# Performance work log

Measured on AMD Instinct MI355X. Metric: run time of the kernel, lower is better.

Reference implementation:

```python
import jax, jax.numpy as jnp
import numpy as np

# Mamba2(d_model=256, headdim=32) defaults: d_state=128, d_conv=4, expand=2, ngroups=1, chunk=256
B, CIN, L = 8, 256, 1024
D_MODEL = CIN
D_INNER = 2 * D_MODEL            # expand=2 -> 512
HEADDIM = 32
NHEADS = D_INNER // HEADDIM      # 16
D_STATE = 128
D_CONV = 4
CONV_DIM = D_INNER + 2 * D_STATE             # 768 (ngroups=1)
D_IN_PROJ = 2 * D_INNER + 2 * D_STATE + NHEADS  # 1296
GN_GROUPS = 8
CHUNK = 256
EPS = 1e-5

def setup_inputs():
    key = jax.random.key(0)
    ks = jax.random.split(key, 8)
    x = jax.random.normal(ks[0], (B, CIN, L), jnp.float32)
    W_in = jax.random.normal(ks[1], (D_IN_PROJ, D_MODEL), jnp.float32) * 0.02
    conv_w = jax.random.normal(ks[2], (CONV_DIM, D_CONV), jnp.float32) * 0.2
    conv_b = jax.random.normal(ks[3], (CONV_DIM,), jnp.float32) * 0.02
    dt = jnp.exp(jax.random.uniform(ks[4], (NHEADS,)) * (jnp.log(0.1) - jnp.log(0.001)) + jnp.log(0.001))
    dt_bias = dt + jnp.log(-jnp.expm1(-dt))   # inverse softplus
    A_log = jnp.log(jax.random.uniform(ks[5], (NHEADS,), minval=1.0, maxval=16.0))
    Dp = jnp.ones((NHEADS,), jnp.float32)
    rms_w = jnp.ones((D_INNER,), jnp.float32)
    W_out = jax.random.normal(ks[6], (D_MODEL, D_INNER), jnp.float32) * 0.02
    gn_w = jnp.ones((CIN,), jnp.float32)
    gn_b = jnp.zeros((CIN,), jnp.float32)
    return dict(x=x, W_in=W_in, conv_w=conv_w, conv_b=conv_b, dt_bias=dt_bias,
                A_log=A_log, Dp=Dp, rms_w=rms_w, W_out=W_out, gn_w=gn_w, gn_b=gn_b)

def segsum(a):
    # a: (..., T) -> (..., T, T) with sum_{j<i<=t} a_i on/below diagonal, -inf above
    T = a.shape[-1]
    cs = jnp.cumsum(a, -1)
    d = cs[..., :, None] - cs[..., None, :]
    mask = jnp.tril(jnp.ones((T, T), bool))
    return jnp.where(mask, d, -jnp.inf)

def ssd(X, A, Bm, Cm):
    # X: (b,l,h,p) already dt-scaled; A: (b,l,h) = dt*A_cont; Bm,Cm: (b,l,n) (ngroups=1)
    b, l, h, p = X.shape
    n = Bm.shape[-1]
    c = l // CHUNK
    X = X.reshape(b, c, CHUNK, h, p)
    A = A.reshape(b, c, CHUNK, h).transpose(0, 3, 1, 2)      # (b,h,c,l)
    Bm = Bm.reshape(b, c, CHUNK, n)
    Cm = Cm.reshape(b, c, CHUNK, n)
    A_cs = jnp.cumsum(A, -1)                                  # (b,h,c,l)
    Lmat = jnp.exp(segsum(A))                                 # (b,h,c,l,l)
    Y_diag = jnp.einsum('bcln,bcsn,bhcls,bcshp->bclhp', Cm, Bm, Lmat, X)
    decay_states = jnp.exp(A_cs[..., -1:] - A_cs)             # (b,h,c,l)
    states = jnp.einsum('bcln,bhcl,bclhp->bchpn', Bm, decay_states, X)
    decay_chunk = jnp.exp(segsum(jnp.pad(A_cs[..., -1], ((0, 0), (0, 0), (1, 0)))))  # (b,h,c+1,c+1)
    states = jnp.concatenate([jnp.zeros_like(states[:, :1]), states], axis=1)        # (b,c+1,h,p,n)
    prev = jnp.einsum('bhzc,bchpn->bzhpn', decay_chunk, states)[:, :-1]              # (b,c,h,p,n)
    Y_off = jnp.einsum('bcln,bchpn,bhcl->bclhp', Cm, prev, jnp.exp(A_cs))
    return (Y_diag + Y_off).reshape(b, l, h, p)

def _forward(x, W_in, conv_w, conv_b, dt_bias, A_log, Dp, rms_w, W_out, gn_w, gn_b):
    u = jnp.transpose(x, (0, 2, 1))                           # (B,L,d_model)
    zxbcdt = u @ W_in.T                                       # (B,L,1296)
    z = zxbcdt[..., :D_INNER]
    xBC = zxbcdt[..., D_INNER:D_INNER + CONV_DIM]
    dt = jax.nn.softplus(zxbcdt[..., D_INNER + CONV_DIM:] + dt_bias)  # (B,L,H)
    # causal depthwise conv1d + SiLU
    xpad = jnp.pad(xBC, ((0, 0), (D_CONV - 1, 0), (0, 0)))
    xconv = conv_b + sum(conv_w[:, k] * xpad[:, k:k + L, :] for k in range(D_CONV))
    xconv = jax.nn.silu(xconv)
    xs = xconv[..., :D_INNER].reshape(B, L, NHEADS, HEADDIM)
    Bm = xconv[..., D_INNER:D_INNER + D_STATE]
    Cm = xconv[..., D_INNER + D_STATE:]
    A = -jnp.exp(A_log)                                       # (H,)
    Y = ssd(dt[..., None] * xs, dt * A, Bm, Cm)               # (B,L,H,P)
    Y = Y + xs * Dp[None, None, :, None]
    # gated RMSNorm (norm_before_gate=False): rmsnorm(y * silu(z)) * weight
    y = Y.reshape(B, L, D_INNER) * jax.nn.silu(z)
    y = y * jax.lax.rsqrt(jnp.mean(y * y, -1, keepdims=True) + EPS) * rms_w
    out = jnp.transpose(y @ W_out.T, (0, 2, 1))               # (B,C,L)
    # GroupNorm(8, C) over (channels_per_group, L)
    og = out.reshape(B, GN_GROUPS, CIN // GN_GROUPS, L)
    mu = og.mean((2, 3), keepdims=True)
    var = og.var((2, 3), keepdims=True)
    out = ((og - mu) * jax.lax.rsqrt(var + EPS)).reshape(B, CIN, L)
    out = out * gn_w[None, :, None] + gn_b[None, :, None]
    return out * jnp.tanh(jax.nn.softplus(out))               # Mish

def reference(x, W_in, conv_w, conv_b, dt_bias, A_log, Dp, rms_w, W_out, gn_w, gn_b):
    return _forward(x, W_in, conv_w, conv_b, dt_bias, A_log, Dp, rms_w, W_out, gn_w, gn_b)
```

## Files before the change

kernel.cpp:

```cpp
#include <hip/hip_runtime.h>
#include <hip/hip_bf16.h>
#include <math.h>

#define B_ 8
#define L_ 1024
#define DM 256
#define DI 512
#define HD 32
#define NH 16
#define DS 128
#define CDIM 768
#define NZX 1280
#define CH 256
#define NC 4
#define M_ (B_*L_)
#define EPSV 1e-5f

typedef short bf16x8 __attribute__((ext_vector_type(8)));
typedef float f32x4 __attribute__((ext_vector_type(4)));

#define OFF_ZX   0
#define SZ_ZX    (M_*NZX/2)
#define OFF_XC   (OFF_ZX+SZ_ZX)
#define SZ_XC    (M_*CDIM/2)
#define OFF_DT   (OFF_XC+SZ_XC)
#define SZ_DT    (M_*NH)
#define OFF_ACS  (OFF_DT+SZ_DT)
#define SZ_ACS   (B_*NC*NH*CH)
#define OFF_S0   (OFF_ACS+SZ_ACS)
#define SZ_S0    (B_*NC*CH*CH/2)
#define OFF_ST   (OFF_S0+SZ_S0)
#define SZ_ST    (B_*NC*NH*HD*DS)
#define OFF_PV   (OFF_ST+SZ_ST)
#define SZ_PV    SZ_ST
#define OFF_Y    (OFF_PV+SZ_PV)
#define SZ_Y     (M_*DI/2)
#define OFF_YNB  (OFF_Y+SZ_Y)
#define SZ_YNB   (M_*DI/2)
#define OFF_XBF  (OFF_YNB+SZ_YNB)
#define SZ_XBF   (M_*DM/2)
#define OFF_WBF  (OFF_XBF+SZ_XBF)
#define SZ_WBF   (1296*DM/2)
#define OFF_WOBF (OFF_WBF+SZ_WBF)
#define SZ_WOBF  (DM*DI/2)
#define OFF_GNP  (OFF_WOBF+SZ_WOBF)
#define SZ_GNP   (64*2)
#define OFF_BT   (OFF_GNP+SZ_GNP)
#define SZ_BT    (32*128*256/2)

__device__ __forceinline__ ushort f2bf(float v) {
  __hip_bfloat16 h = __float2bfloat16(v);
  return *(ushort*)&h;
}
__device__ __forceinline__ float bf2f(ushort u) {
  return __uint_as_float(((unsigned int)u) << 16);
}

__global__ void k_zero_gnp(float2* __restrict__ gnp) {
  gnp[threadIdx.x] = make_float2(0.f, 0.f);
}

__global__ void k_cast(const float* __restrict__ s, ushort* __restrict__ d, int n) {
  int i = blockIdx.x*256 + threadIdx.x;
  if (i < n) d[i] = f2bf(s[i]);
}

__global__ __launch_bounds__(256) void k_cast_x(const float* __restrict__ x,
                                                ushort* __restrict__ xbf) {
  __shared__ float Ts[64][65];
  const int k0 = blockIdx.x*64, l0 = blockIdx.y*64, b = blockIdx.z;
  const int t = threadIdx.x;
  for (int i = t; i < 4096; i += 256) {
    int kk = i>>6, ll = i&63;
    Ts[kk][ll] = x[(size_t)b*DM*L_ + (size_t)(k0+kk)*L_ + l0+ll];
  }
  __syncthreads();
  for (int i = t; i < 4096; i += 256) {
    int mm = i>>6, kk = i&63;
    xbf[(size_t)(b*L_ + l0+mm)*DM + k0+kk] = f2bf(Ts[kk][mm]);
  }
}

__global__ __launch_bounds__(256) void k_xpose(const ushort* __restrict__ xcb,
                                               ushort* __restrict__ dst,
                                               int src_col0, int ncols) {
  __shared__ ushort T[64][66];
  const int c0 = blockIdx.x*64, l0 = blockIdx.y*64, bc = blockIdx.z;
  const int t = threadIdx.x;
  const int base = bc*CH;
  for (int i = t; i < 4096; i += 256) {
    int lr = i>>6, cc = i&63;
    T[lr][cc] = xcb[(size_t)(base+l0+lr)*CDIM + src_col0 + c0+cc];
  }
  __syncthreads();
  for (int i = t; i < 4096; i += 256) {
    int cc = i>>6, lr = i&63;
    dst[((size_t)bc*ncols + c0+cc)*CH + l0+lr] = T[lr][cc];
  }
}

__global__ __launch_bounds__(256) void k_gemm_in_mfma(const ushort* __restrict__ xbf,
                                                      const ushort* __restrict__ wbf,
                                                      ushort* __restrict__ zxb) {
  __shared__ ushort As[128*40];
  __shared__ ushort Bs[64*40];
  const int tid = threadIdx.x;
  const int n0 = blockIdx.x*64, m0 = blockIdx.y*128;
  const int wave = tid>>6, lane = tid&63;
  const int lr = lane&15, quad = lane>>4;
  const int KK = DM;
  f32x4 acc[2][4];
#pragma unroll
  for (int mi=0;mi<2;++mi)
#pragma unroll
    for (int ni=0;ni<4;++ni)
#pragma unroll
      for (int r=0;r<4;++r) acc[mi][ni][r] = 0.f;
  const int srow = tid>>2, sc = tid&3;
  for (int k0 = 0; k0 < KK; k0 += 32) {
    *(uint4*)&As[srow*40 + sc*8]      = *(const uint4*)(xbf + (size_t)(m0+srow)*KK    + k0 + sc*8);
    *(uint4*)&As[(srow+64)*40 + sc*8] = *(const uint4*)(xbf + (size_t)(m0+srow+64)*KK + k0 + sc*8);
    *(uint4*)&Bs[srow*40 + sc*8]      = *(const uint4*)(wbf + (size_t)(n0+srow)*KK    + k0 + sc*8);
    __syncthreads();
    bf16x8 af[2], bfr[4];
    const int ar = wave*32 + lr;
    af[0] = *(const bf16x8*)&As[ar*40 + quad*8];
    af[1] = *(const bf16x8*)&As[(ar+16)*40 + quad*8];
#pragma unroll
    for (int ni=0;ni<4;++ni) bfr[ni] = *(const bf16x8*)&Bs[(ni*16+lr)*40 + quad*8];
#pragma unroll
    for (int mi=0;mi<2;++mi)
#pragma unroll
      for (int ni=0;ni<4;++ni)
        acc[mi][ni] = __builtin_amdgcn_mfma_f32_16x16x32_bf16(af[mi], bfr[ni], acc[mi][ni], 0, 0, 0);
    __syncthreads();
  }
#pragma unroll
  for (int mi=0;mi<2;++mi) {
    int m = m0 + wave*32 + mi*16 + quad*4;
#pragma unroll
    for (int ni=0;ni<4;++ni) {
      int n = n0 + ni*16 + lr;
#pragma unroll
      for (int r=0;r<4;++r) zxb[(size_t)(m+r)*NZX + n] = f2bf(acc[mi][ni][r]);
    }
  }
}

__global__ __launch_bounds__(256) void k_dt_direct(const float* __restrict__ x,
                                                   const float* __restrict__ W,
                                                   const float* __restrict__ dt_bias,
                                                   float* __restrict__ dtb) {
  __shared__ float Xs[256][16];
  __shared__ float Ws[16][257];
  const int t = threadIdx.x;
  const int bm = blockIdx.x*16;
  const int b = bm >> 10, l0 = bm & 1023;
  for (int i = t; i < 4096; i += 256) {
    int h = i>>8, k = i&255;
    Ws[h][k] = W[(size_t)(NZX+h)*DM + k];
  }
  for (int i = t; i < 4096; i += 256) {
    int k = i>>4, li = i&15;
    Xs[k][li] = x[(size_t)b*DM*L_ + (size_t)k*L_ + l0+li];
  }
  __syncthreads();
  const int h = t&15, li = t>>4;
  float acc = 0.f;
#pragma unroll 8
  for (int k = 0; k < 256; ++k) acc += Xs[k][li]*Ws[h][k];
  float v = acc + dt_bias[h];
  dtb[(size_t)bm*NH + t] = (v > 20.f) ? v : log1pf(expf(v));
}

__global__ __launch_bounds__(256) void k_conv(const ushort* __restrict__ zxb,
                                              const float* __restrict__ cw,
                                              const float* __restrict__ cb,
                                              ushort* __restrict__ xcb) {
  const int j = blockIdx.x*256 + threadIdx.x;
  const int l0 = (blockIdx.y*4) & 1023;
  const int mb = (blockIdx.y*4) & ~1023;
  const float4 w = *(const float4*)&cw[j*4];
  const float bias = cb[j];
  float v[7];
#pragma unroll
  for (int i = 0; i < 7; ++i) {
    int ll = l0 - 3 + i;
    v[i] = (ll >= 0) ? bf2f(zxb[(size_t)(mb+ll)*NZX + DI + j]) : 0.f;
  }
#pragma unroll
  for (int i = 0; i < 4; ++i) {
    float a = bias + w.x*v[i] + w.y*v[i+1] + w.z*v[i+2] + w.w*v[i+3];
    a = a / (1.f + expf(-a));
    xcb[(size_t)(mb+l0+i)*CDIM + j] = f2bf(a);
  }
}

__global__ __launch_bounds__(256) void k_s0_mfma(const ushort* __restrict__ xcb,
                                                 ushort* __restrict__ S0b) {
  const int lt = blockIdx.x, st = blockIdx.y, bc = blockIdx.z;
  if (st > lt) return;
  const int base = bc*CH;
  const int t = threadIdx.x;
  const int wave = t>>6, lane = t&63, lr = lane&15, quad = lane>>4;
  const int l = lt*64 + wave*16 + lr;
  f32x4 acc[4];
#pragma unroll
  for (int nt = 0; nt < 4; ++nt)
#pragma unroll
    for (int r = 0; r < 4; ++r) acc[nt][r] = 0.f;
#pragma unroll
  for (int ks = 0; ks < 4; ++ks) {
    bf16x8 af = *(const bf16x8*)(xcb + (size_t)(base+l)*CDIM + (DI+DS) + ks*32 + quad*8);
#pragma unroll
    for (int nt = 0; nt < 4; ++nt) {
      bf16x8 bf = *(const bf16x8*)(xcb + (size_t)(base + st*64 + nt*16 + lr)*CDIM + DI + ks*32 + quad*8);
      acc[nt] = __builtin_amdgcn_mfma_f32_16x16x32_bf16(af, bf, acc[nt], 0, 0, 0);
    }
  }
#pragma unroll
  for (int nt = 0; nt < 4; ++nt)
#pragma unroll
    for (int r = 0; r < 4; ++r)
      S0b[((size_t)bc*CH + lt*64 + wave*16 + quad*4 + r)*CH + st*64 + nt*16 + lr] = f2bf(acc[nt][r]);
}

__global__ __launch_bounds__(256) void k_states_mfma(const ushort* __restrict__ xcb,
                                                     const ushort* __restrict__ btg,
                                                     const float* __restrict__ dtb,
                                                     const float* __restrict__ A_log,
                                                     float* __restrict__ acs_g,
                                                     float* __restrict__ st) {
  __shared__ float acs[CH];
  __shared__ ushort Xw[32][264];
  const int t = threadIdx.x;
  const int bc = blockIdx.x, h = blockIdx.y;
  const int base = bc*CH;
  float dt_t = dtb[(size_t)(base+t)*NH + h];
  float An = -expf(A_log[h]);
  acs[t] = dt_t * An;
  __syncthreads();
  for (int off = 1; off < CH; off <<= 1) {
    float v = (t >= off) ? acs[t-off] : 0.f;
    __syncthreads();
    acs[t] += v;
    __syncthreads();
  }
  float alast = acs[CH-1];
  acs_g[((size_t)bc*NH + h)*CH + t] = acs[t];
  float w = expf(alast - acs[t]) * dt_t;
  {
    const ushort* xp = xcb + (size_t)(base+t)*CDIM + h*HD;
    ushort tmp[32];
    *(uint4*)&tmp[0]  = *(const uint4*)(xp);
    *(uint4*)&tmp[8]  = *(const uint4*)(xp+8);
    *(uint4*)&tmp[16] = *(const uint4*)(xp+16);
    *(uint4*)&tmp[24] = *(const uint4*)(xp+24);
#pragma unroll
    for (int p = 0; p < 32; ++p) Xw[p][t] = f2bf(bf2f(tmp[p]) * w);
  }
  __syncthreads();
  const int wave = t>>6, lane = t&63, lr = lane&15, quad = lane>>4;
  f32x4 acc[2][2];
#pragma unroll
  for (int mt=0;mt<2;++mt)
#pragma unroll
    for (int nt=0;nt<2;++nt)
#pragma unroll
      for (int r=0;r<4;++r) acc[mt][nt][r] = 0.f;
  const ushort* bp = btg + (size_t)bc*DS*CH;
#pragma unroll
  for (int k0 = 0; k0 < CH; k0 += 32) {
    bf16x8 a0 = *(const bf16x8*)&Xw[lr][k0 + quad*8];
    bf16x8 a1 = *(const bf16x8*)&Xw[16+lr][k0 + quad*8];
    bf16x8 b0 = *(const bf16x8*)(bp + (size_t)(wave*32 + lr)*CH + k0 + quad*8);
    bf16x8 b1 = *(const bf16x8*)(bp + (size_t)(wave*32 + 16 + lr)*CH + k0 + quad*8);
    acc[0][0] = __builtin_amdgcn_mfma_f32_16x16x32_bf16(a0, b0, acc[0][0], 0,0,0);
    acc[0][1] = __builtin_amdgcn_mfma_f32_16x16x32_bf16(a0, b1, acc[0][1], 0,0,0);
    acc[1][0] = __builtin_amdgcn_mfma_f32_16x16x32_bf16(a1, b0, acc[1][0], 0,0,0);
    acc[1][1] = __builtin_amdgcn_mfma_f32_16x16x32_bf16(a1, b1, acc[1][1], 0,0,0);
  }
  size_t sb = ((size_t)bc*NH + h)*HD*DS;
#pragma unroll
  for (int mt = 0; mt < 2; ++mt)
#pragma unroll
    for (int nt = 0; nt < 2; ++nt)
#pragma unroll
      for (int r = 0; r < 4; ++r)
        st[sb + (size_t)(mt*16 + quad*4 + r)*DS + wave*32 + nt*16 + lr] = acc[mt][nt][r];
}

__global__ void k_scan(const float* __restrict__ acs_g, const float* __restrict__ st,
                       float* __restrict__ pv) {
  const int b = blockIdx.x, h = blockIdx.y;
  const int t = threadIdx.x;
  float P[16];
#pragma unroll
  for (int i = 0; i < 16; ++i) P[i] = 0.f;
  for (int c = 0; c < NC; ++c) {
    size_t sb = ((size_t)(b*NC+c)*NH + h)*HD*DS;
    float T = acs_g[((size_t)(b*NC+c)*NH + h)*CH + (CH-1)];
    float ec = expf(T);
#pragma unroll
    for (int i = 0; i < 16; ++i) {
      size_t e = sb + (size_t)i*256 + t;
      pv[e] = P[i];
      P[i] = st[e] + ec * P[i];
    }
  }
}

__global__ __launch_bounds__(256) void k_y_mfma(const ushort* __restrict__ xcb,
    const float* __restrict__ dtb, const float* __restrict__ acs_g,
    const ushort* __restrict__ S0b, const float* __restrict__ pv,
    const float* __restrict__ Dp, ushort* __restrict__ Yb) {
  __shared__ ushort Xt[32][280];
  __shared__ float acs[CH];
  __shared__ float dts[CH];
  __shared__ float E8[CH];
  const int t = threadIdx.x;
  const int bc = blockIdx.x, h = blockIdx.y;
  const int base = bc*CH;
  acs[t] = acs_g[((size_t)bc*NH + h)*CH + t];
  dts[t] = dtb[(size_t)(base+t)*NH + h];
  {
    const ushort* xp = xcb + (size_t)(base+t)*CDIM + h*HD;
    ushort tmp[32];
    *(uint4*)&tmp[0]  = *(const uint4*)(xp);
    *(uint4*)&tmp[8]  = *(const uint4*)(xp+8);
    *(uint4*)&tmp[16] = *(const uint4*)(xp+16);
    *(uint4*)&tmp[24] = *(const uint4*)(xp+24);
#pragma unroll
    for (int p = 0; p < 32; ++p) Xt[p][t] = tmp[p];
  }
  __syncthreads();
  E8[t] = expf(acs[t & ~7] - acs[t]) * dts[t];
  __syncthreads();
  const int wave = t>>6, lane = t&63, lr = lane&15, quad = lane>>4;
  f32x4 acc[4][2];
#pragma unroll
  for (int mt=0;mt<4;++mt)
#pragma unroll
    for (int nt=0;nt<2;++nt)
#pragma unroll
      for (int r=0;r<4;++r) acc[mt][nt][r] = 0.f;
  const size_t pb = ((size_t)bc*NH + h)*HD*DS;
#pragma unroll
  for (int ks = 0; ks < 4; ++ks) {
    bf16x8 bfr[2];
#pragma unroll
    for (int nt = 0; nt < 2; ++nt) {
      const float* pp = pv + pb + (size_t)(nt*16+lr)*DS + ks*32 + quad*8;
      float4 v0 = *(const float4*)pp;
      float4 v1 = *(const float4*)(pp+4);
      bf16x8 bb;
      bb[0]=(short)f2bf(v0.x); bb[1]=(short)f2bf(v0.y); bb[2]=(short)f2bf(v0.z); bb[3]=(short)f2bf(v0.w);
      bb[4]=(short)f2bf(v1.x); bb[5]=(short)f2bf(v1.y); bb[6]=(short)f2bf(v1.z); bb[7]=(short)f2bf(v1.w);
      bfr[nt] = bb;
    }
#pragma unroll
    for (int mt = 0; mt < 4; ++mt) {
      int l = wave*64 + mt*16 + lr;
      bf16x8 af = *(const bf16x8*)(xcb + (size_t)(base+l)*CDIM + (DI+DS) + ks*32 + quad*8);
      acc[mt][0] = __builtin_amdgcn_mfma_f32_16x16x32_bf16(af, bfr[0], acc[mt][0], 0,0,0);
      acc[mt][1] = __builtin_amdgcn_mfma_f32_16x16x32_bf16(af, bfr[1], acc[mt][1], 0,0,0);
    }
  }
#pragma unroll
  for (int mt = 0; mt < 4; ++mt)
#pragma unroll
    for (int r = 0; r < 4; ++r) {
      float e = expf(acs[wave*64 + mt*16 + quad*4 + r]);
      acc[mt][0][r] *= e;
      acc[mt][1][r] *= e;
    }
  float al[4];
#pragma unroll
  for (int mt = 0; mt < 4; ++mt) al[mt] = acs[wave*64 + mt*16 + lr];
  const int km3 = 2*wave + 1;
  for (int ks = 0; ks <= km3; ++ks) {
    const int sq = ks*32 + quad*8;
    const float as0 = acs[sq];
    const float4 e0 = *(const float4*)&E8[sq];
    const float4 e1 = *(const float4*)&E8[sq+4];
    const bf16x8 xb0 = *(const bf16x8*)&Xt[lr][sq];
    const bf16x8 xb1 = *(const bf16x8*)&Xt[16+lr][sq];
    const float ev[8] = {e0.x,e0.y,e0.z,e0.w,e1.x,e1.y,e1.z,e1.w};
#pragma unroll
    for (int mt = 0; mt < 4; ++mt) {
      if (ks > ((wave*64 + mt*16 + 15) >> 5)) continue;
      const int l = wave*64 + mt*16 + lr;
      const bf16x8 sb = *(const bf16x8*)(S0b + ((size_t)bc*CH + l)*CH + sq);
      const float el = expf(al[mt] - as0);
      bf16x8 mf;
#pragma unroll
      for (int j = 0; j < 8; ++j) {
        float v = (sq + j <= l) ? bf2f((ushort)sb[j]) * el * ev[j] : 0.f;
        mf[j] = (short)f2bf(v);
      }
      acc[mt][0] = __builtin_amdgcn_mfma_f32_16x16x32_bf16(mf, xb0, acc[mt][0], 0,0,0);
      acc[mt][1] = __builtin_amdgcn_mfma_f32_16x16x32_bf16(mf, xb1, acc[mt][1], 0,0,0);
    }
  }
  const float dph = Dp[h];
#pragma unroll
  for (int mt = 0; mt < 4; ++mt) {
    const int lb = wave*64 + mt*16 + quad*4;
#pragma unroll
    for (int nt = 0; nt < 2; ++nt) {
      const int p = nt*16 + lr;
#pragma unroll
      for (int r = 0; r < 4; ++r) {
        float xv = bf2f(Xt[p][lb+r]);
        Yb[(size_t)(base+lb+r)*DI + h*HD + p] = f2bf(acc[mt][nt][r] + dph*xv);
      }
    }
  }
}

__global__ __launch_bounds__(256) void k_rms(const ushort* __restrict__ zxb,
                                             const ushort* __restrict__ Yb,
                                             const float* __restrict__ rw,
                                             ushort* __restrict__ yn) {
  const int m = blockIdx.x, t = threadIdx.x;
  float z0 = bf2f(zxb[(size_t)m*NZX + t]);
  float z1 = bf2f(zxb[(size_t)m*NZX + t + 256]);
  float y0 = bf2f(Yb[(size_t)m*DI + t])       * z0 / (1.f + expf(-z0));
  float y1 = bf2f(Yb[(size_t)m*DI + t + 256]) * z1 / (1.f + expf(-z1));
  float ss = y0*y0 + y1*y1;
#pragma unroll
  for (int off = 32; off > 0; off >>= 1) ss += __shfl_down(ss, off);
  __shared__ float red[4];
  __shared__ float sinv;
  if ((t & 63) == 0) red[t >> 6] = ss;
  __syncthreads();
  if (t == 0) sinv = rsqrtf((red[0]+red[1]+red[2]+red[3]) * (1.f/DI) + EPSV);
  __syncthreads();
  float inv = sinv;
  yn[(size_t)m*DI + t]       = f2bf(y0 * inv * rw[t]);
  yn[(size_t)m*DI + t + 256] = f2bf(y1 * inv * rw[t+256]);
}

__global__ __launch_bounds__(256) void k_gemm_out_mfma(const ushort* __restrict__ ynbf,
                                                       const ushort* __restrict__ wobf,
                                                       float* __restrict__ outp,
                                                       float2* __restrict__ gnp) {
  __shared__ ushort As[128*40];
  __shared__ ushort Bs[64*40];
  const int tid = threadIdx.x;
  const int n0 = blockIdx.x*64, m0 = blockIdx.y*128;
  const int wave = tid>>6, lane = tid&63;
  const int lr = lane&15, quad = lane>>4;
  const int KK = DI;
  f32x4 acc[2][4];
#pragma unroll
  for (int mi=0;mi<2;++mi)
#pragma unroll
    for (int ni=0;ni<4;++ni)
#pragma unroll
      for (int r=0;r<4;++r) acc[mi][ni][r] = 0.f;
  const int srow = tid>>2, sc = tid&3;
  for (int k0 = 0; k0 < KK; k0 += 32) {
    *(uint4*)&As[srow*40 + sc*8]      = *(const uint4*)(ynbf + (size_t)(m0+srow)*KK    + k0 + sc*8);
    *(uint4*)&As[(srow+64)*40 + sc*8] = *(const uint4*)(ynbf + (size_t)(m0+srow+64)*KK + k0 + sc*8);
    *(uint4*)&Bs[srow*40 + sc*8]      = *(const uint4*)(wobf + (size_t)(n0+srow)*KK    + k0 + sc*8);
    __syncthreads();
    bf16x8 af[2], bfr[4];
    const int ar = wave*32 + lr;
    af[0] = *(const bf16x8*)&As[ar*40 + quad*8];
    af[1] = *(const bf16x8*)&As[(ar+16)*40 + quad*8];
#pragma unroll
    for (int ni=0;ni<4;++ni) bfr[ni] = *(const bf16x8*)&Bs[(ni*16+lr)*40 + quad*8];
#pragma unroll
    for (int mi=0;mi<2;++mi)
#pragma unroll
      for (int ni=0;ni<4;++ni)
        acc[mi][ni] = __builtin_amdgcn_mfma_f32_16x16x32_bf16(af[mi], bfr[ni], acc[mi][ni], 0, 0, 0);
    __syncthreads();
  }
  const int b = m0 >> 10, l0 = m0 & 1023;
  float s0=0.f, ss0=0.f, s1=0.f, ss1=0.f;
#pragma unroll
  for (int mi=0;mi<2;++mi) {
    int lb = l0 + wave*32 + mi*16 + quad*4;
#pragma unroll
    for (int ni=0;ni<4;++ni) {
      int n = n0 + ni*16 + lr;
      float4 v = make_float4(acc[mi][ni][0], acc[mi][ni][1], acc[mi][ni][2], acc[mi][ni][3]);
      *(float4*)&outp[(size_t)b*DM*L_ + (size_t)n*L_ + lb] = v;
      float ps = v.x+v.y+v.z+v.w;
      float pq = v.x*v.x+v.y*v.y+v.z*v.z+v.w*v.w;
      if (ni < 2) { s0 += ps; ss0 += pq; } else { s1 += ps; ss1 += pq; }
    }
  }
#pragma unroll
  for (int off = 32; off > 0; off >>= 1) {
    s0 += __shfl_down(s0, off); ss0 += __shfl_down(ss0, off);
    s1 += __shfl_down(s1, off); ss1 += __shfl_down(ss1, off);
  }
  __shared__ float red[4][4];
  if (lane == 0) { red[wave][0]=s0; red[wave][1]=ss0; red[wave][2]=s1; red[wave][3]=ss1; }
  __syncthreads();
  if (tid == 0) {
    float S0=0,Q0=0,S1=0,Q1=0;
#pragma unroll
    for (int wv2 = 0; wv2 < 4; ++wv2) { S0+=red[wv2][0]; Q0+=red[wv2][1]; S1+=red[wv2][2]; Q1+=red[wv2][3]; }
    int g0 = b*8 + (n0>>5);
    atomicAdd(&gnp[g0].x, S0);   atomicAdd(&gnp[g0].y, Q0);
    atomicAdd(&gnp[g0+1].x, S1); atomicAdd(&gnp[g0+1].y, Q1);
  }
}

__global__ __launch_bounds__(256) void k_gn_apply(const float2* __restrict__ gnp,
                                                  const float* __restrict__ gw,
                                                  const float* __restrict__ gb,
                                                  float* __restrict__ o) {
  const int ch = blockIdx.x & 255, b = blockIdx.x >> 8;
  const int t = threadIdx.x;
  float2 p = gnp[b*8 + (ch>>5)];
  const float mean = p.x * (1.f/(32.f*L_));
  const float var  = p.y * (1.f/(32.f*L_)) - mean*mean;
  const float inv  = rsqrtf(var + EPSV);
  const float w = gw[ch], bb = gb[ch];
  size_t base = (size_t)blockIdx.x * L_;
  float4 v = *(const float4*)&o[base + t*4];
  float r[4] = {v.x, v.y, v.z, v.w};
#pragma unroll
  for (int j = 0; j < 4; ++j) {
    float u = (r[j] - mean) * inv * w + bb;
    float m;
    if (u > 15.f) m = u;
    else {
      float e = expf(u);
      float a = 1.f + e;
      float a2 = a*a;
      m = u * (a2 - 1.f) / (a2 + 1.f);
    }
    r[j] = m;
  }
  *(float4*)&o[base + t*4] = make_float4(r[0], r[1], r[2], r[3]);
}

extern "C" void kernel_launch(void* const* d_in, const int* in_sizes, int n_in,
                              void* d_out, int out_size, void* d_ws, size_t ws_size,
                              hipStream_t stream) {
  const float* x       = (const float*)d_in[0];
  const float* W_in    = (const float*)d_in[1];
  const float* conv_w  = (const float*)d_in[2];
  const float* conv_b  = (const float*)d_in[3];
  const float* dt_bias = (const float*)d_in[4];
  const float* A_log   = (const float*)d_in[5];
  const float* Dp      = (const float*)d_in[6];
  const float* rms_w   = (const float*)d_in[7];
  const float* W_out   = (const float*)d_in[8];
  const float* gn_w    = (const float*)d_in[9];
  const float* gn_b    = (const float*)d_in[10];
  float* out = (float*)d_out;
  float* ws  = (float*)d_ws;

  ushort* zxb   = (ushort*)(ws + OFF_ZX);
  ushort* xcb   = (ushort*)(ws + OFF_XC);
  float*  dtb   = ws + OFF_DT;
  float*  acs   = ws + OFF_ACS;
  ushort* S0b   = (ushort*)(ws + OFF_S0);
  float*  st    = ws + OFF_ST;
  float*  pv    = ws + OFF_PV;
  ushort* Ybb   = (ushort*)(ws + OFF_Y);
  ushort* ynbf  = (ushort*)(ws + OFF_YNB);
  ushort* xbf   = (ushort*)(ws + OFF_XBF);
  ushort* wbf   = (ushort*)(ws + OFF_WBF);
  ushort* wobf  = (ushort*)(ws + OFF_WOBF);
  float2* gnp   = (float2*)(ws + OFF_GNP);
  ushort* btg   = (ushort*)(ws + OFF_BT);

  k_zero_gnp     <<<dim3(1), 64, 0, stream>>>(gnp);
  k_cast_x       <<<dim3(4, 16, 8), 256, 0, stream>>>(x, xbf);
  k_cast         <<<dim3((1296*DM+255)/256), 256, 0, stream>>>(W_in, wbf, 1296*DM);
  k_cast         <<<dim3((DM*DI+255)/256), 256, 0, stream>>>(W_out, wobf, DM*DI);
  k_gemm_in_mfma <<<dim3(NZX/64, M_/128), 256, 0, stream>>>(xbf, wbf, zxb);
  k_dt_direct    <<<dim3(M_/16), 256, 0, stream>>>(x, W_in, dt_bias, dtb);
  k_conv         <<<dim3(3, M_/4), 256, 0, stream>>>(zxb, conv_w, conv_b, xcb);
  k_xpose        <<<dim3(2, 4, B_*NC), 256, 0, stream>>>(xcb, btg, DI, DS);
  k_s0_mfma      <<<dim3(4, 4, B_*NC), 256, 0, stream>>>(xcb, S0b);
  k_states_mfma  <<<dim3(B_*NC, NH), 256, 0, stream>>>(xcb, btg, dtb, A_log, acs, st);
  k_scan         <<<dim3(B_, NH), 256, 0, stream>>>(acs, st, pv);
  k_y_mfma       <<<dim3(B_*NC, NH), 256, 0, stream>>>(xcb, dtb, acs, S0b, pv, Dp, Ybb);
  k_rms          <<<dim3(M_), 256, 0, stream>>>(zxb, Ybb, rms_w, ynbf);
  k_gemm_out_mfma<<<dim3(DM/64, M_/128), 256, 0, stream>>>(ynbf, wobf, out, gnp);
  k_gn_apply     <<<dim3(B_*DM), 256, 0, stream>>>(gnp, gn_w, gn_b, out);
}
```

Baseline: 197.4 us.

## Merge prep casts into one kernel, fuse B transpose into conv, bf16 GEMM-out intermediate

Combines the zeroing, x transpose-cast and the two weight casts into a single launch. Folds the B-matrix transpose into the conv kernel, which now handles 8 timesteps per thread and writes a packed uint4 per channel. Has the out-projection GEMM store a bf16 intermediate for GroupNorm to read instead of fp32, halving that traffic at some cost in precision before normalization. Together these remove three kernel launches and some memory round trips.

```diff
diff --git a/kernel.cpp b/kernel.cpp
--- a/kernel.cpp
+++ b/kernel.cpp
@@ -47,6 +47,8 @@
 #define SZ_GNP   (64*2)
 #define OFF_BT   (OFF_GNP+SZ_GNP)
 #define SZ_BT    (32*128*256/2)
+#define OFF_OUTB (OFF_BT+SZ_BT)
+#define SZ_OUTB  (M_*DM/2)
 
 __device__ __forceinline__ ushort f2bf(float v) {
   __hip_bfloat16 h = __float2bfloat16(v);
@@ -56,46 +58,36 @@
   return __uint_as_float(((unsigned int)u) << 16);
 }
 
-__global__ void k_zero_gnp(float2* __restrict__ gnp) {
-  gnp[threadIdx.x] = make_float2(0.f, 0.f);
-}
-
-__global__ void k_cast(const float* __restrict__ s, ushort* __restrict__ d, int n) {
-  int i = blockIdx.x*256 + threadIdx.x;
-  if (i < n) d[i] = f2bf(s[i]);
-}
-
-__global__ __launch_bounds__(256) void k_cast_x(const float* __restrict__ x,
-                                                ushort* __restrict__ xbf) {
+__global__ __launch_bounds__(256) void k_prep(const float* __restrict__ x,
+                                              const float* __restrict__ W_in,
+                                              const float* __restrict__ W_out,
+                                              ushort* __restrict__ xbf,
+                                              ushort* __restrict__ wbf,
+                                              ushort* __restrict__ wobf,
+                                              float2* __restrict__ gnp) {
   __shared__ float Ts[64][65];
-  const int k0 = blockIdx.x*64, l0 = blockIdx.y*64, b = blockIdx.z;
-  const int t = threadIdx.x;
-  for (int i = t; i < 4096; i += 256) {
-    int kk = i>>6, ll = i&63;
-    Ts[kk][ll] = x[(size_t)b*DM*L_ + (size_t)(k0+kk)*L_ + l0+ll];
-  }
-  __syncthreads();
-  for (int i = t; i < 4096; i += 256) {
-    int mm = i>>6, kk = i&63;
-    xbf[(size_t)(b*L_ + l0+mm)*DM + k0+kk] = f2bf(Ts[kk][mm]);
-  }
-}
-
-__global__ __launch_bounds__(256) void k_xpose(const ushort* __restrict__ xcb,
-                                               ushort* __restrict__ dst,
-                                               int src_col0, int ncols) {
-  __shared__ ushort T[64][66];
-  const int c0 = blockIdx.x*64, l0 = blockIdx.y*64, bc = blockIdx.z;
-  const int t = threadIdx.x;
-  const int base = bc*CH;
-  for (int i = t; i < 4096; i += 256) {
-    int lr = i>>6, cc = i&63;
-    T[lr][cc] = xcb[(size_t)(base+l0+lr)*CDIM + src_col0 + c0+cc];
-  }
-  __syncthreads();
-  for (int i = t; i < 4096; i += 256) {
-    int cc = i>>6, lr = i&63;
-    dst[((size_t)bc*ncols + c0+cc)*CH + l0+lr] = T[lr][cc];
+  const int bid = blockIdx.x;
+  const int t = threadIdx.x;
+  if (bid < 512) {
+    const int kt = bid & 3, lt = (bid >> 2) & 15, b = bid >> 6;
+    const int k0 = kt*64, l0 = lt*64;
+    for (int i = t; i < 4096; i += 256) {
+      int kk = i>>6, ll = i&63;
+      Ts[kk][ll] = x[(size_t)b*DM*L_ + (size_t)(k0+kk)*L_ + l0+ll];
+    }
+    __syncthreads();
+    for (int i = t; i < 4096; i += 256) {
+      int mm = i>>6, kk = i&63;
+      xbf[(size_t)(b*L_ + l0+mm)*DM + k0+kk] = f2bf(Ts[kk][mm]);
+    }
+  } else if (bid < 512 + 1296) {
+    int i = (bid-512)*256 + t;
+    if (i < 1296*DM) wbf[i] = f2bf(W_in[i]);
+  } else if (bid < 512 + 1296 + 512) {
+    int i = (bid-512-1296)*256 + t;
+    wobf[i] = f2bf(W_out[i]);
+  } else {
+    if (t < 64) gnp[t] = make_float2(0.f, 0.f);
   }
 }
 
@@ -176,23 +168,33 @@
 __global__ __launch_bounds__(256) void k_conv(const ushort* __restrict__ zxb,
                                               const float* __restrict__ cw,
                                               const float* __restrict__ cb,
-                                              ushort* __restrict__ xcb) {
+                                              ushort* __restrict__ xcb,
+                                              ushort* __restrict__ btg) {
   const int j = blockIdx.x*256 + threadIdx.x;
-  const int l0 = (blockIdx.y*4) & 1023;
-  const int mb = (blockIdx.y*4) & ~1023;
+  const int m8 = blockIdx.y*8;
+  const int l0 = m8 & 1023;
+  const int mb = m8 & ~1023;
   const float4 w = *(const float4*)&cw[j*4];
   const float bias = cb[j];
-  float v[7];
-#pragma unroll
-  for (int i = 0; i < 7; ++i) {
+  float v[11];
+#pragma unroll
+  for (int i = 0; i < 11; ++i) {
     int ll = l0 - 3 + i;
     v[i] = (ll >= 0) ? bf2f(zxb[(size_t)(mb+ll)*NZX + DI + j]) : 0.f;
   }
-#pragma unroll
-  for (int i = 0; i < 4; ++i) {
+  union { ushort u[8]; uint4 q; } res;
+#pragma unroll
+  for (int i = 0; i < 8; ++i) {
     float a = bias + w.x*v[i] + w.y*v[i+1] + w.z*v[i+2] + w.w*v[i+3];
     a = a / (1.f + expf(-a));
-    xcb[(size_t)(mb+l0+i)*CDIM + j] = f2bf(a);
+    res.u[i] = f2bf(a);
+    xcb[(size_t)(mb+l0+i)*CDIM + j] = res.u[i];
+  }
+  if (j >= DI && j < DI+DS) {
+    const int n = j - DI;
+    const int bc = (mb >> 10)*NC + (l0 >> 8);
+    const int lc = l0 & 255;
+    *(uint4*)&btg[((size_t)bc*DS + n)*CH + lc] = res.q;
   }
 }
 
@@ -443,7 +445,7 @@
 
 __global__ __launch_bounds__(256) void k_gemm_out_mfma(const ushort* __restrict__ ynbf,
                                                        const ushort* __restrict__ wobf,
-                                                       float* __restrict__ outp,
+                                                       ushort* __restrict__ outb,
                                                        float2* __restrict__ gnp) {
   __shared__ ushort As[128*40];
   __shared__ ushort Bs[64*40];
@@ -486,10 +488,13 @@
 #pragma unroll
     for (int ni=0;ni<4;++ni) {
       int n = n0 + ni*16 + lr;
-      float4 v = make_float4(acc[mi][ni][0], acc[mi][ni][1], acc[mi][ni][2], acc[mi][ni][3]);
-      *(float4*)&outp[(size_t)b*DM*L_ + (size_t)n*L_ + lb] = v;
-      float ps = v.x+v.y+v.z+v.w;
-      float pq = v.x*v.x+v.y*v.y+v.z*v.z+v.w*v.w;
+      union { ushort u[4]; uint2 q; } pk;
+#pragma unroll
+      for (int r=0;r<4;++r) pk.u[r] = f2bf(acc[mi][ni][r]);
+      *(uint2*)&outb[(size_t)b*DM*L_ + (size_t)n*L_ + lb] = pk.q;
+      float ps = acc[mi][ni][0]+acc[mi][ni][1]+acc[mi][ni][2]+acc[mi][ni][3];
+      float pq = acc[mi][ni][0]*acc[mi][ni][0]+acc[mi][ni][1]*acc[mi][ni][1]
+               + acc[mi][ni][2]*acc[mi][ni][2]+acc[mi][ni][3]*acc[mi][ni][3];
       if (ni < 2) { s0 += ps; ss0 += pq; } else { s1 += ps; ss1 += pq; }
     }
   }
@@ -514,6 +519,7 @@
 __global__ __launch_bounds__(256) void k_gn_apply(const float2* __restrict__ gnp,
                                                   const float* __restrict__ gw,
                                                   const float* __restrict__ gb,
+                                                  const ushort* __restrict__ ob,
                                                   float* __restrict__ o) {
   const int ch = blockIdx.x & 255, b = blockIdx.x >> 8;
   const int t = threadIdx.x;
@@ -523,8 +529,8 @@
   const float inv  = rsqrtf(var + EPSV);
   const float w = gw[ch], bb = gb[ch];
   size_t base = (size_t)blockIdx.x * L_;
-  float4 v = *(const float4*)&o[base + t*4];
-  float r[4] = {v.x, v.y, v.z, v.w};
+  ushort4 v = *(const ushort4*)&ob[base + t*4];
+  float r[4] = {bf2f(v.x), bf2f(v.y), bf2f(v.z), bf2f(v.w)};
 #pragma unroll
   for (int j = 0; j < 4; ++j) {
     float u = (r[j] - mean) * inv * w + bb;
@@ -572,20 +578,17 @@
   ushort* wobf  = (ushort*)(ws + OFF_WOBF);
   float2* gnp   = (float2*)(ws + OFF_GNP);
   ushort* btg   = (ushort*)(ws + OFF_BT);
-
-  k_zero_gnp     <<<dim3(1), 64, 0, stream>>>(gnp);
-  k_cast_x       <<<dim3(4, 16, 8), 256, 0, stream>>>(x, xbf);
-  k_cast         <<<dim3((1296*DM+255)/256), 256, 0, stream>>>(W_in, wbf, 1296*DM);
-  k_cast         <<<dim3((DM*DI+255)/256), 256, 0, stream>>>(W_out, wobf, DM*DI);
+  ushort* outb  = (ushort*)(ws + OFF_OUTB);
+
+  k_prep         <<<dim3(512+1296+512+1), 256, 0, stream>>>(x, W_in, W_out, xbf, wbf, wobf, gnp);
   k_gemm_in_mfma <<<dim3(NZX/64, M_/128), 256, 0, stream>>>(xbf, wbf, zxb);
   k_dt_direct    <<<dim3(M_/16), 256, 0, stream>>>(x, W_in, dt_bias, dtb);
-  k_conv         <<<dim3(3, M_/4), 256, 0, stream>>>(zxb, conv_w, conv_b, xcb);
-  k_xpose        <<<dim3(2, 4, B_*NC), 256, 0, stream>>>(xcb, btg, DI, DS);
+  k_conv         <<<dim3(3, M_/8), 256, 0, stream>>>(zxb, conv_w, conv_b, xcb, btg);
   k_s0_mfma      <<<dim3(4, 4, B_*NC), 256, 0, stream>>>(xcb, S0b);
   k_states_mfma  <<<dim3(B_*NC, NH), 256, 0, stream>>>(xcb, btg, dtb, A_log, acs, st);
   k_scan         <<<dim3(B_, NH), 256, 0, stream>>>(acs, st, pv);
   k_y_mfma       <<<dim3(B_*NC, NH), 256, 0, stream>>>(xcb, dtb, acs, S0b, pv, Dp, Ybb);
   k_rms          <<<dim3(M_), 256, 0, stream>>>(zxb, Ybb, rms_w, ynbf);
-  k_gemm_out_mfma<<<dim3(DM/64, M_/128), 256, 0, stream>>>(ynbf, wobf, out, gnp);
-  k_gn_apply     <<<dim3(B_*DM), 256, 0, stream>>>(gnp, gn_w, gn_b, out);
-}
+  k_gemm_out_mfma<<<dim3(DM/64, M_/128), 256, 0, stream>>>(ynbf, wobf, outb, gnp);
+  k_gn_apply     <<<dim3(B_*DM), 256, 0, stream>>>(gnp, gn_w, gn_b, outb, out);
+}
```

New measurement: 191.9 us. 2.8% less time.
